# Kernel optimization log

Measured on AMD Instinct MI355X. Metric: run time of the kernel, lower is better.

The kernel has to match this reference:

```python
import jax, jax.numpy as jnp
import numpy as np

B, I, H = 32768, 1024, 1024

def _xavier(key, shape):
    fan_out, fan_in = shape
    limit = float(np.sqrt(6.0 / (fan_in + fan_out)))
    return jax.random.uniform(key, shape, jnp.float32, -limit, limit)

def setup_inputs() -> dict:
    key = jax.random.key(0)
    ks = jax.random.split(key, 8)
    return {
        "x": jax.random.normal(ks[0], (B, I), jnp.float32),
        "h": jax.random.normal(ks[1], (B, H), jnp.float32),
        "weight_ir": _xavier(ks[2], (H, I)),
        "weight_hr": _xavier(ks[3], (H, H)),
        "weight_iz": _xavier(ks[4], (H, I)),
        "weight_hz": _xavier(ks[5], (H, H)),
        "weight_in": _xavier(ks[6], (H, I)),
        "weight_hn": _xavier(ks[7], (H, H)),
        "bias_ir": jnp.zeros((H,), jnp.float32),
        "bias_hr": jnp.zeros((H,), jnp.float32),
        "bias_iz": jnp.zeros((H,), jnp.float32),
        "bias_hz": jnp.zeros((H,), jnp.float32),
        "bias_in": jnp.zeros((H,), jnp.float32),
        "bias_hn": jnp.zeros((H,), jnp.float32),
    }

def reference(x, h, weight_ir, weight_hr, weight_iz, weight_hz, weight_in, weight_hn,
              bias_ir, bias_hr, bias_iz, bias_hz, bias_in, bias_hn):
    # Fuse the 3 input-side and 3 hidden-side GEMMs into two concatenated GEMMs
    # (same math as 6 separate F.linear calls).
    Wi = jnp.concatenate([weight_ir, weight_iz, weight_in], axis=0)  # [3H, I]
    Wh = jnp.concatenate([weight_hr, weight_hz, weight_hn], axis=0)  # [3H, H]
    bi = jnp.concatenate([bias_ir, bias_iz, bias_in])
    bh = jnp.concatenate([bias_hr, bias_hz, bias_hn])
    gi = x @ Wi.T + bi   # [B, 3H]
    gh = h @ Wh.T + bh   # [B, 3H]
    Hd = weight_hr.shape[0]
    ir, iz, inn = gi[:, :Hd], gi[:, Hd:2*Hd], gi[:, 2*Hd:]
    hr, hz, hn = gh[:, :Hd], gh[:, Hd:2*Hd], gh[:, 2*Hd:]
    r = jax.nn.sigmoid(ir + hr)
    z = jax.nn.sigmoid(iz + hz)
    n = jnp.tanh(inn + r * hn)
    return (1.0 - z) * n + z * h
```

## Files before the change

### kernel.cpp

```cpp
#include <hip/hip_runtime.h>
#include <hip/hip_bf16.h>


#define B_ROWS 32768
#define KD     1024
#define HD     1024

#define BM 128
#define BN 64
#define BK 32

typedef __bf16 bf16_t;
typedef __bf16 bf16x8 __attribute__((ext_vector_type(8)));
typedef __bf16 bf16x4 __attribute__((ext_vector_type(4)));
typedef float  f32x4  __attribute__((ext_vector_type(4)));

#define XT_BYTES  67108864ull
#define WT_OFF   134217728ull
#define WS_NEEDED 146800640ull

#define X_SLOTS 4194304
#define W_BASE_SLOT 8388608
#define TOTAL_SLOTS 9175040

__device__ __forceinline__ float sigm_f(float v) { return 1.0f / (1.0f + __expf(-v)); }
__device__ __forceinline__ float tanh_f(float v) { return 2.0f / (1.0f + __expf(-2.0f * v)) - 1.0f; }

__device__ __forceinline__ bf16x4 cvt4(f32x4 v) {
    bf16x4 r;
    r[0] = (bf16_t)v[0]; r[1] = (bf16_t)v[1];
    r[2] = (bf16_t)v[2]; r[3] = (bf16_t)v[3];
    return r;
}

__device__ __forceinline__ void glds16(const void* g, void* l) {
    __builtin_amdgcn_global_load_lds(
        (const __attribute__((address_space(1))) void*)g,
        (__attribute__((address_space(3))) void*)l, 16, 0, 0);
}

struct WPtrs { const float* p[6]; };

__global__ void __launch_bounds__(256)
cvt_kernel(const float* __restrict__ x, const float* __restrict__ h,
           WPtrs wp, bf16_t* __restrict__ ws)
{
    int sid = blockIdx.x * 256 + threadIdx.x;
    if (sid >= TOTAL_SLOTS) return;

    const float* src;
    if (sid < W_BASE_SLOT) {
        const float* base = (sid < X_SLOTS) ? x : h;
        int s2   = sid & (X_SLOTS - 1);
        int tile = s2 >> 9;
        int c    = s2 & 511;
        int row  = c >> 2, s = c & 3;
        int mt   = tile >> 5, kt = tile & 31;
        int ks   = s ^ ((row >> 1) & 3);
        src = base + (size_t)(mt * 128 + row) * KD + kt * 32 + ks * 8;
    } else {
        int s2   = sid - W_BASE_SLOT;
        int tile = s2 / 1536;
        int c    = s2 % 1536;
        int g    = c >> 8;
        int cc   = c & 255;
        int row  = cc >> 2, s = cc & 3;
        int nt   = tile >> 5, kt = tile & 31;
        int ks   = s ^ ((row >> 1) & 3);
        src = wp.p[g] + (size_t)(nt * 64 + row) * KD + kt * 32 + ks * 8;
    }
    f32x4 a = *(const f32x4*)src;
    f32x4 b = *(const f32x4*)(src + 4);
    bf16x8 o;
    o[0]=(bf16_t)a[0]; o[1]=(bf16_t)a[1]; o[2]=(bf16_t)a[2]; o[3]=(bf16_t)a[3];
    o[4]=(bf16_t)b[0]; o[5]=(bf16_t)b[1]; o[6]=(bf16_t)b[2]; o[7]=(bf16_t)b[3];
    *(bf16x8*)(ws + (size_t)sid * 8) = o;
}

__global__ void __launch_bounds__(256, 2)
gru_mfma_kernel(const bf16_t* __restrict__ xt, const bf16_t* __restrict__ ht,
                const bf16_t* __restrict__ wt,
                const float* __restrict__ h,
                const float* __restrict__ b_ir, const float* __restrict__ b_hr,
                const float* __restrict__ b_iz, const float* __restrict__ b_hz,
                const float* __restrict__ b_in, const float* __restrict__ b_hn,
                float* __restrict__ out)
{
    __shared__ __align__(16) char smem[2][40960];

    const int tid  = threadIdx.x;
    const int lane = tid & 63;
    const int wid  = tid >> 6;
    const int wr   = wid >> 1;
    const int wc   = wid & 1;

    const int nblk = HD / BN;
    const int bidN = blockIdx.x % nblk;
    const int bidM = blockIdx.x / nblk;
    const int rowBase = bidM * BM;
    const int colBase = bidN * BN;

    const char* xcb = (const char*)xt + (size_t)bidM * 32 * 8192;
    const char* hcb = (const char*)ht + (size_t)bidM * 32 * 8192;
    const char* wcb = (const char*)wt + (size_t)bidN * 32 * 24576;

    const f32x4 vzero = {0.f, 0.f, 0.f, 0.f};
    f32x4 accR[4][2], accZ[4][2], accIN[4][2], accHN[4][2];
    #pragma unroll
    for (int m = 0; m < 4; ++m)
        #pragma unroll
        for (int n = 0; n < 2; ++n) {
            accR[m][n] = vzero; accZ[m][n] = vzero;
            accIN[m][n] = vzero; accHN[m][n] = vzero;
        }

    const int fr  = lane & 15;
    const int sl  = lane >> 4;
    const int f   = (fr >> 1) & 3;
    const int col = ((sl ^ f) << 4);
    int aoff[4], boff[2];
    #pragma unroll
    for (int m = 0; m < 4; ++m) aoff[m] = (wr * 64 + m * 16 + fr) * 64 + col;
    #pragma unroll
    for (int n = 0; n < 2; ++n) boff[n] = (wc * 32 + n * 16 + fr) * 64 + col;

    auto STAGE = [&](int buf, int kt) {
        const char* xc  = xcb + (size_t)kt * 8192;
        const char* hc  = hcb + (size_t)kt * 8192;
        const char* wc2 = wcb + (size_t)kt * 24576;
        char* s = smem[buf];
        #pragma unroll
        for (int i = 0; i < 2; ++i) {
            int off = wid * 2048 + i * 1024;
            glds16(xc + off + lane * 16, s + off);
            glds16(hc + off + lane * 16, s + 8192 + off);
        }
        #pragma unroll
        for (int j = 0; j < 6; ++j) {
            int off = wid * 6144 + j * 1024;
            glds16(wc2 + off + lane * 16, s + 16384 + off);
        }
    };

    auto COMPUTE = [&](const char* s) {
        bf16x8 xa[4], ha[4];
        #pragma unroll
        for (int m = 0; m < 4; ++m) {
            xa[m] = *(const bf16x8*)(s + aoff[m]);
            ha[m] = *(const bf16x8*)(s + 8192 + aoff[m]);
        }
        bf16x8 w0[2], w1[2];
        #pragma unroll
        for (int n = 0; n < 2; ++n) {
            w0[n] = *(const bf16x8*)(s + 16384 + 0 * 4096 + boff[n]);
            w1[n] = *(const bf16x8*)(s + 16384 + 1 * 4096 + boff[n]);
        }
        __builtin_amdgcn_s_setprio(1);
        #pragma unroll
        for (int m = 0; m < 4; ++m)
            #pragma unroll
            for (int n = 0; n < 2; ++n) {
                accR[m][n] = __builtin_amdgcn_mfma_f32_16x16x32_bf16(xa[m], w0[n], accR[m][n], 0, 0, 0);
                accR[m][n] = __builtin_amdgcn_mfma_f32_16x16x32_bf16(ha[m], w1[n], accR[m][n], 0, 0, 0);
            }
        __builtin_amdgcn_s_setprio(0);
        bf16x8 w2[2], w3[2];
        #pragma unroll
        for (int n = 0; n < 2; ++n) {
            w2[n] = *(const bf16x8*)(s + 16384 + 2 * 4096 + boff[n]);
            w3[n] = *(const bf16x8*)(s + 16384 + 3 * 4096 + boff[n]);
        }
        __builtin_amdgcn_s_setprio(1);
        #pragma unroll
        for (int m = 0; m < 4; ++m)
            #pragma unroll
            for (int n = 0; n < 2; ++n) {
                accZ[m][n] = __builtin_amdgcn_mfma_f32_16x16x32_bf16(xa[m], w2[n], accZ[m][n], 0, 0, 0);
                accZ[m][n] = __builtin_amdgcn_mfma_f32_16x16x32_bf16(ha[m], w3[n], accZ[m][n], 0, 0, 0);
            }
        __builtin_amdgcn_s_setprio(0);
        bf16x8 w4[2], w5[2];
        #pragma unroll
        for (int n = 0; n < 2; ++n) {
            w4[n] = *(const bf16x8*)(s + 16384 + 4 * 4096 + boff[n]);
            w5[n] = *(const bf16x8*)(s + 16384 + 5 * 4096 + boff[n]);
        }
        __builtin_amdgcn_s_setprio(1);
        #pragma unroll
        for (int m = 0; m < 4; ++m)
            #pragma unroll
            for (int n = 0; n < 2; ++n) {
                accIN[m][n] = __builtin_amdgcn_mfma_f32_16x16x32_bf16(xa[m], w4[n], accIN[m][n], 0, 0, 0);
                accHN[m][n] = __builtin_amdgcn_mfma_f32_16x16x32_bf16(ha[m], w5[n], accHN[m][n], 0, 0, 0);
            }
        __builtin_amdgcn_s_setprio(0);
    };

    STAGE(0, 0);

    for (int kt = 0; kt < 31; ++kt) {
        STAGE((kt + 1) & 1, kt + 1);
        asm volatile("s_waitcnt vmcnt(10)" ::: "memory");
        __builtin_amdgcn_s_barrier();
        __builtin_amdgcn_sched_barrier(0);
        COMPUTE(smem[kt & 1]);
        __builtin_amdgcn_sched_barrier(0);
        __builtin_amdgcn_s_barrier();
    }
    asm volatile("s_waitcnt vmcnt(0)" ::: "memory");
    __builtin_amdgcn_s_barrier();
    __builtin_amdgcn_sched_barrier(0);
    COMPUTE(smem[1]);

    const int rq = (lane >> 4) * 4;
    float br[2], bz[2], bi[2], bh[2];
    #pragma unroll
    for (int n = 0; n < 2; ++n) {
        int c = colBase + wc * 32 + n * 16 + fr;
        br[n] = b_ir[c] + b_hr[c];
        bz[n] = b_iz[c] + b_hz[c];
        bi[n] = b_in[c];
        bh[n] = b_hn[c];
    }
    #pragma unroll
    for (int m = 0; m < 4; ++m) {
        #pragma unroll
        for (int n = 0; n < 2; ++n) {
            int gc = colBase + wc * 32 + n * 16 + fr;
            #pragma unroll
            for (int j = 0; j < 4; ++j) {
                int gr = rowBase + wr * 64 + m * 16 + rq + j;
                float rv = sigm_f(accR[m][n][j] + br[n]);
                float zv = sigm_f(accZ[m][n][j] + bz[n]);
                float nv = tanh_f(accIN[m][n][j] + bi[n] + rv * (accHN[m][n][j] + bh[n]));
                float hv = h[(size_t)gr * HD + gc];
                out[(size_t)gr * HD + gc] = (1.0f - zv) * nv + zv * hv;
            }
        }
    }
}

#define PK 40
__global__ void __launch_bounds__(256, 2)
gru_fused_kernel(const float* __restrict__ x,  const float* __restrict__ h,
                 const float* __restrict__ w_ir, const float* __restrict__ w_hr,
                 const float* __restrict__ w_iz, const float* __restrict__ w_hz,
                 const float* __restrict__ w_in, const float* __restrict__ w_hn,
                 const float* __restrict__ b_ir, const float* __restrict__ b_hr,
                 const float* __restrict__ b_iz, const float* __restrict__ b_hz,
                 const float* __restrict__ b_in, const float* __restrict__ b_hn,
                 float* __restrict__ out)
{
    __shared__ __align__(16) bf16_t xs[BM][PK];
    __shared__ __align__(16) bf16_t hs[BM][PK];
    __shared__ __align__(16) bf16_t ws[6][BN][PK];

    const int tid  = threadIdx.x;
    const int lane = tid & 63;
    const int wid  = tid >> 6;
    const int wr   = wid >> 1;
    const int wc   = wid & 1;

    const int nblk = HD / BN;
    const int bidN = blockIdx.x % nblk;
    const int bidM = blockIdx.x / nblk;
    const int rowBase = bidM * BM;
    const int colBase = bidN * BN;

    const float* wptr[6] = { w_ir, w_hr, w_iz, w_hz, w_in, w_hn };

    int sr[4], sc[4];
    #pragma unroll
    for (int i = 0; i < 4; ++i) {
        int idx = tid + i * 256;
        sr[i] = idx >> 3;
        sc[i] = (idx & 7) * 4;
    }
    int xoff[4];
    #pragma unroll
    for (int i = 0; i < 4; ++i) xoff[i] = (rowBase + sr[i]) * KD + sc[i];
    int woff[2];
    #pragma unroll
    for (int i = 0; i < 2; ++i) woff[i] = (colBase + sr[i]) * KD + sc[i];

    const f32x4 vzero = {0.f, 0.f, 0.f, 0.f};
    f32x4 accR[4][2], accZ[4][2], accIN[4][2], accHN[4][2];
    #pragma unroll
    for (int m = 0; m < 4; ++m)
        #pragma unroll
        for (int n = 0; n < 2; ++n) {
            accR[m][n] = vzero; accZ[m][n] = vzero;
            accIN[m][n] = vzero; accHN[m][n] = vzero;
        }

    const int fr = lane & 15;
    const int ko = (lane >> 4) * 8;

    for (int k0 = 0; k0 < KD; k0 += BK) {
        __syncthreads();
        #pragma unroll
        for (int i = 0; i < 4; ++i) {
            f32x4 vx = *(const f32x4*)&x[xoff[i] + k0];
            f32x4 vh = *(const f32x4*)&h[xoff[i] + k0];
            *(bf16x4*)&xs[sr[i]][sc[i]] = cvt4(vx);
            *(bf16x4*)&hs[sr[i]][sc[i]] = cvt4(vh);
        }
        #pragma unroll
        for (int g = 0; g < 6; ++g) {
            #pragma unroll
            for (int i = 0; i < 2; ++i) {
                f32x4 vw = *(const f32x4*)&wptr[g][woff[i] + k0];
                *(bf16x4*)&ws[g][sr[i]][sc[i]] = cvt4(vw);
            }
        }
        __syncthreads();

        bf16x8 xa[4], ha[4];
        #pragma unroll
        for (int m = 0; m < 4; ++m) {
            xa[m] = *(const bf16x8*)&xs[wr * 64 + m * 16 + fr][ko];
            ha[m] = *(const bf16x8*)&hs[wr * 64 + m * 16 + fr][ko];
        }
        bf16x8 wb[6][2];
        #pragma unroll
        for (int g = 0; g < 6; ++g)
            #pragma unroll
            for (int n = 0; n < 2; ++n)
                wb[g][n] = *(const bf16x8*)&ws[g][wc * 32 + n * 16 + fr][ko];

        #pragma unroll
        for (int m = 0; m < 4; ++m) {
            #pragma unroll
            for (int n = 0; n < 2; ++n) {
                accR[m][n]  = __builtin_amdgcn_mfma_f32_16x16x32_bf16(xa[m], wb[0][n], accR[m][n], 0, 0, 0);
                accR[m][n]  = __builtin_amdgcn_mfma_f32_16x16x32_bf16(ha[m], wb[1][n], accR[m][n], 0, 0, 0);
                accZ[m][n]  = __builtin_amdgcn_mfma_f32_16x16x32_bf16(xa[m], wb[2][n], accZ[m][n], 0, 0, 0);
                accZ[m][n]  = __builtin_amdgcn_mfma_f32_16x16x32_bf16(ha[m], wb[3][n], accZ[m][n], 0, 0, 0);
                accIN[m][n] = __builtin_amdgcn_mfma_f32_16x16x32_bf16(xa[m], wb[4][n], accIN[m][n], 0, 0, 0);
                accHN[m][n] = __builtin_amdgcn_mfma_f32_16x16x32_bf16(ha[m], wb[5][n], accHN[m][n], 0, 0, 0);
            }
        }
    }

    const int rq = (lane >> 4) * 4;
    float br[2], bz[2], bi[2], bh[2];
    #pragma unroll
    for (int n = 0; n < 2; ++n) {
        int c = colBase + wc * 32 + n * 16 + fr;
        br[n] = b_ir[c] + b_hr[c];
        bz[n] = b_iz[c] + b_hz[c];
        bi[n] = b_in[c];
        bh[n] = b_hn[c];
    }
    #pragma unroll
    for (int m = 0; m < 4; ++m) {
        #pragma unroll
        for (int n = 0; n < 2; ++n) {
            int gc = colBase + wc * 32 + n * 16 + fr;
            #pragma unroll
            for (int j = 0; j < 4; ++j) {
                int gr = rowBase + wr * 64 + m * 16 + rq + j;
                float rv = sigm_f(accR[m][n][j] + br[n]);
                float zv = sigm_f(accZ[m][n][j] + bz[n]);
                float nv = tanh_f(accIN[m][n][j] + bi[n] + rv * (accHN[m][n][j] + bh[n]));
                float hv = h[gr * HD + gc];
                out[gr * HD + gc] = (1.0f - zv) * nv + zv * hv;
            }
        }
    }
}

extern "C" void kernel_launch(void* const* d_in, const int* in_sizes, int n_in,
                              void* d_out, int out_size, void* d_ws, size_t ws_size,
                              hipStream_t stream) {
    const float* x    = (const float*)d_in[0];
    const float* h    = (const float*)d_in[1];
    const float* w_ir = (const float*)d_in[2];
    const float* w_hr = (const float*)d_in[3];
    const float* w_iz = (const float*)d_in[4];
    const float* w_hz = (const float*)d_in[5];
    const float* w_in = (const float*)d_in[6];
    const float* w_hn = (const float*)d_in[7];
    const float* b_ir = (const float*)d_in[8];
    const float* b_hr = (const float*)d_in[9];
    const float* b_iz = (const float*)d_in[10];
    const float* b_hz = (const float*)d_in[11];
    const float* b_in = (const float*)d_in[12];
    const float* b_hn = (const float*)d_in[13];
    float* out = (float*)d_out;

    if (ws_size >= WS_NEEDED) {
        bf16_t* ws = (bf16_t*)d_ws;
        WPtrs wp;
        wp.p[0] = w_ir; wp.p[1] = w_hr; wp.p[2] = w_iz;
        wp.p[3] = w_hz; wp.p[4] = w_in; wp.p[5] = w_hn;
        cvt_kernel<<<(TOTAL_SLOTS + 255) / 256, 256, 0, stream>>>(x, h, wp, ws);

        const bf16_t* xt = ws;
        const bf16_t* ht = ws + XT_BYTES / 2;
        const bf16_t* wt = ws + WT_OFF / 2;
        dim3 grid((B_ROWS / BM) * (HD / BN));
        gru_mfma_kernel<<<grid, 256, 0, stream>>>(
            xt, ht, wt, h, b_ir, b_hr, b_iz, b_hz, b_in, b_hn, out);
    } else {
        dim3 grid((B_ROWS / BM) * (HD / BN));
        gru_fused_kernel<<<grid, 256, 0, stream>>>(
            x, h, w_ir, w_hr, w_iz, w_hz, w_in, w_hn,
            b_ir, b_hr, b_iz, b_hz, b_in, b_hn, out);
    }
}
```

Baseline: 477.4 us.

## Widen MFMA GRU tile to 128x128 with 8 waves and inner-loop barriers

Doubles the N tile of the bf16 MFMA GRU kernel to 128 columns and runs it with 512 threads (8 waves, 2x4 layout), so each staged x/h tile is reused across twice as many output columns and global traffic for the activations is halved. The weight pre-conversion layout is changed to match the 128-row weight tiles. The compute body is inlined into the loop, with explicit lgkmcnt waits and extra workgroup barriers between the gate phases. The trade-off is 128KB of LDS per block, one block per CU, and more barriers, which lowers latency hiding and occupancy.

```diff
diff --git a/kernel.cpp b/kernel.cpp
--- a/kernel.cpp
+++ b/kernel.cpp
@@ -7,7 +7,7 @@
 #define HD     1024
 
 #define BM 128
-#define BN 64
+#define BN 128
 #define BK 32
 
 typedef __bf16 bf16_t;
@@ -60,14 +60,14 @@
         src = base + (size_t)(mt * 128 + row) * KD + kt * 32 + ks * 8;
     } else {
         int s2   = sid - W_BASE_SLOT;
-        int tile = s2 / 1536;
-        int c    = s2 % 1536;
-        int g    = c >> 8;
-        int cc   = c & 255;
+        int tile = s2 / 3072;
+        int c    = s2 % 3072;
+        int g    = c >> 9;
+        int cc   = c & 511;
         int row  = cc >> 2, s = cc & 3;
         int nt   = tile >> 5, kt = tile & 31;
         int ks   = s ^ ((row >> 1) & 3);
-        src = wp.p[g] + (size_t)(nt * 64 + row) * KD + kt * 32 + ks * 8;
+        src = wp.p[g] + (size_t)(nt * 128 + row) * KD + kt * 32 + ks * 8;
     }
     f32x4 a = *(const f32x4*)src;
     f32x4 b = *(const f32x4*)(src + 4);
@@ -77,7 +77,7 @@
     *(bf16x8*)(ws + (size_t)sid * 8) = o;
 }
 
-__global__ void __launch_bounds__(256, 2)
+__global__ void __launch_bounds__(512, 1)
 gru_mfma_kernel(const bf16_t* __restrict__ xt, const bf16_t* __restrict__ ht,
                 const bf16_t* __restrict__ wt,
                 const float* __restrict__ h,
@@ -86,13 +86,13 @@
                 const float* __restrict__ b_in, const float* __restrict__ b_hn,
                 float* __restrict__ out)
 {
-    __shared__ __align__(16) char smem[2][40960];
+    __shared__ __align__(16) char smem[2][65536];
 
     const int tid  = threadIdx.x;
     const int lane = tid & 63;
     const int wid  = tid >> 6;
-    const int wr   = wid >> 1;
-    const int wc   = wid & 1;
+    const int wrM  = wid >> 2;
+    const int wcN  = wid & 3;
 
     const int nblk = HD / BN;
     const int bidN = blockIdx.x % nblk;
@@ -102,7 +102,7 @@
 
     const char* xcb = (const char*)xt + (size_t)bidM * 32 * 8192;
     const char* hcb = (const char*)ht + (size_t)bidM * 32 * 8192;
-    const char* wcb = (const char*)wt + (size_t)bidN * 32 * 24576;
+    const char* wcb = (const char*)wt + (size_t)bidN * 32 * 49152;
 
     const f32x4 vzero = {0.f, 0.f, 0.f, 0.f};
     f32x4 accR[4][2], accZ[4][2], accIN[4][2], accHN[4][2];
@@ -120,29 +120,32 @@
     const int col = ((sl ^ f) << 4);
     int aoff[4], boff[2];
     #pragma unroll
-    for (int m = 0; m < 4; ++m) aoff[m] = (wr * 64 + m * 16 + fr) * 64 + col;
-    #pragma unroll
-    for (int n = 0; n < 2; ++n) boff[n] = (wc * 32 + n * 16 + fr) * 64 + col;
+    for (int m = 0; m < 4; ++m) aoff[m] = (wrM * 64 + m * 16 + fr) * 64 + col;
+    #pragma unroll
+    for (int n = 0; n < 2; ++n) boff[n] = (wcN * 32 + n * 16 + fr) * 64 + col;
 
     auto STAGE = [&](int buf, int kt) {
         const char* xc  = xcb + (size_t)kt * 8192;
         const char* hc  = hcb + (size_t)kt * 8192;
-        const char* wc2 = wcb + (size_t)kt * 24576;
+        const char* wc2 = wcb + (size_t)kt * 49152;
         char* s = smem[buf];
-        #pragma unroll
-        for (int i = 0; i < 2; ++i) {
-            int off = wid * 2048 + i * 1024;
-            glds16(xc + off + lane * 16, s + off);
-            glds16(hc + off + lane * 16, s + 8192 + off);
-        }
-        #pragma unroll
-        for (int j = 0; j < 6; ++j) {
-            int off = wid * 6144 + j * 1024;
-            glds16(wc2 + off + lane * 16, s + 16384 + off);
-        }
+        const int wo = wid * 1024;
+        glds16(xc + wo + lane * 16, s + wo);
+        glds16(hc + wo + lane * 16, s + 8192 + wo);
+        #pragma unroll
+        for (int g = 0; g < 6; ++g)
+            glds16(wc2 + g * 8192 + wo + lane * 16, s + 16384 + g * 8192 + wo);
     };
 
-    auto COMPUTE = [&](const char* s) {
+    STAGE(0, 0);
+
+    for (int kt = 0; kt < 31; ++kt) {
+        STAGE((kt + 1) & 1, kt + 1);
+        asm volatile("s_waitcnt vmcnt(8)" ::: "memory");
+        __builtin_amdgcn_s_barrier();
+        __builtin_amdgcn_sched_barrier(0);
+        const char* s = smem[kt & 1];
+
         bf16x8 xa[4], ha[4];
         #pragma unroll
         for (int m = 0; m < 4; ++m) {
@@ -152,9 +155,11 @@
         bf16x8 w0[2], w1[2];
         #pragma unroll
         for (int n = 0; n < 2; ++n) {
-            w0[n] = *(const bf16x8*)(s + 16384 + 0 * 4096 + boff[n]);
-            w1[n] = *(const bf16x8*)(s + 16384 + 1 * 4096 + boff[n]);
-        }
+            w0[n] = *(const bf16x8*)(s + 16384 + 0 * 8192 + boff[n]);
+            w1[n] = *(const bf16x8*)(s + 16384 + 1 * 8192 + boff[n]);
+        }
+        asm volatile("s_waitcnt lgkmcnt(0)" ::: "memory");
+        __builtin_amdgcn_sched_barrier(0);
         __builtin_amdgcn_s_setprio(1);
         #pragma unroll
         for (int m = 0; m < 4; ++m)
@@ -164,12 +169,16 @@
                 accR[m][n] = __builtin_amdgcn_mfma_f32_16x16x32_bf16(ha[m], w1[n], accR[m][n], 0, 0, 0);
             }
         __builtin_amdgcn_s_setprio(0);
+        __builtin_amdgcn_s_barrier();
+
         bf16x8 w2[2], w3[2];
         #pragma unroll
         for (int n = 0; n < 2; ++n) {
-            w2[n] = *(const bf16x8*)(s + 16384 + 2 * 4096 + boff[n]);
-            w3[n] = *(const bf16x8*)(s + 16384 + 3 * 4096 + boff[n]);
-        }
+            w2[n] = *(const bf16x8*)(s + 16384 + 2 * 8192 + boff[n]);
+            w3[n] = *(const bf16x8*)(s + 16384 + 3 * 8192 + boff[n]);
+        }
+        asm volatile("s_waitcnt lgkmcnt(0)" ::: "memory");
+        __builtin_amdgcn_sched_barrier(0);
         __builtin_amdgcn_s_setprio(1);
         #pragma unroll
         for (int m = 0; m < 4; ++m)
@@ -179,12 +188,16 @@
                 accZ[m][n] = __builtin_amdgcn_mfma_f32_16x16x32_bf16(ha[m], w3[n], accZ[m][n], 0, 0, 0);
             }
         __builtin_amdgcn_s_setprio(0);
+        __builtin_amdgcn_s_barrier();
+
         bf16x8 w4[2], w5[2];
         #pragma unroll
         for (int n = 0; n < 2; ++n) {
-            w4[n] = *(const bf16x8*)(s + 16384 + 4 * 4096 + boff[n]);
-            w5[n] = *(const bf16x8*)(s + 16384 + 5 * 4096 + boff[n]);
-        }
+            w4[n] = *(const bf16x8*)(s + 16384 + 4 * 8192 + boff[n]);
+            w5[n] = *(const bf16x8*)(s + 16384 + 5 * 8192 + boff[n]);
+        }
+        asm volatile("s_waitcnt lgkmcnt(0)" ::: "memory");
+        __builtin_amdgcn_sched_barrier(0);
         __builtin_amdgcn_s_setprio(1);
         #pragma unroll
         for (int m = 0; m < 4; ++m)
@@ -194,29 +207,45 @@
                 accHN[m][n] = __builtin_amdgcn_mfma_f32_16x16x32_bf16(ha[m], w5[n], accHN[m][n], 0, 0, 0);
             }
         __builtin_amdgcn_s_setprio(0);
-    };
-
-    STAGE(0, 0);
-
-    for (int kt = 0; kt < 31; ++kt) {
-        STAGE((kt + 1) & 1, kt + 1);
-        asm volatile("s_waitcnt vmcnt(10)" ::: "memory");
         __builtin_amdgcn_s_barrier();
-        __builtin_amdgcn_sched_barrier(0);
-        COMPUTE(smem[kt & 1]);
-        __builtin_amdgcn_sched_barrier(0);
+    }
+
+    {
+        asm volatile("s_waitcnt vmcnt(0)" ::: "memory");
         __builtin_amdgcn_s_barrier();
-    }
-    asm volatile("s_waitcnt vmcnt(0)" ::: "memory");
-    __builtin_amdgcn_s_barrier();
-    __builtin_amdgcn_sched_barrier(0);
-    COMPUTE(smem[1]);
+        __builtin_amdgcn_sched_barrier(0);
+        const char* s = smem[1];
+        bf16x8 xa[4], ha[4], wb[6][2];
+        #pragma unroll
+        for (int m = 0; m < 4; ++m) {
+            xa[m] = *(const bf16x8*)(s + aoff[m]);
+            ha[m] = *(const bf16x8*)(s + 8192 + aoff[m]);
+        }
+        #pragma unroll
+        for (int g = 0; g < 6; ++g)
+            #pragma unroll
+            for (int n = 0; n < 2; ++n)
+                wb[g][n] = *(const bf16x8*)(s + 16384 + g * 8192 + boff[n]);
+        asm volatile("s_waitcnt lgkmcnt(0)" ::: "memory");
+        __builtin_amdgcn_sched_barrier(0);
+        #pragma unroll
+        for (int m = 0; m < 4; ++m)
+            #pragma unroll
+            for (int n = 0; n < 2; ++n) {
+                accR[m][n]  = __builtin_amdgcn_mfma_f32_16x16x32_bf16(xa[m], wb[0][n], accR[m][n], 0, 0, 0);
+                accR[m][n]  = __builtin_amdgcn_mfma_f32_16x16x32_bf16(ha[m], wb[1][n], accR[m][n], 0, 0, 0);
+                accZ[m][n]  = __builtin_amdgcn_mfma_f32_16x16x32_bf16(xa[m], wb[2][n], accZ[m][n], 0, 0, 0);
+                accZ[m][n]  = __builtin_amdgcn_mfma_f32_16x16x32_bf16(ha[m], wb[3][n], accZ[m][n], 0, 0, 0);
+                accIN[m][n] = __builtin_amdgcn_mfma_f32_16x16x32_bf16(xa[m], wb[4][n], accIN[m][n], 0, 0, 0);
+                accHN[m][n] = __builtin_amdgcn_mfma_f32_16x16x32_bf16(ha[m], wb[5][n], accHN[m][n], 0, 0, 0);
+            }
+    }
 
     const int rq = (lane >> 4) * 4;
     float br[2], bz[2], bi[2], bh[2];
     #pragma unroll
     for (int n = 0; n < 2; ++n) {
-        int c = colBase + wc * 32 + n * 16 + fr;
+        int c = colBase + wcN * 32 + n * 16 + fr;
         br[n] = b_ir[c] + b_hr[c];
         bz[n] = b_iz[c] + b_hz[c];
         bi[n] = b_in[c];
@@ -226,10 +255,10 @@
     for (int m = 0; m < 4; ++m) {
         #pragma unroll
         for (int n = 0; n < 2; ++n) {
-            int gc = colBase + wc * 32 + n * 16 + fr;
+            int gc = colBase + wcN * 32 + n * 16 + fr;
             #pragma unroll
             for (int j = 0; j < 4; ++j) {
-                int gr = rowBase + wr * 64 + m * 16 + rq + j;
+                int gr = rowBase + wrM * 64 + m * 16 + rq + j;
                 float rv = sigm_f(accR[m][n][j] + br[n]);
                 float zv = sigm_f(accZ[m][n][j] + bz[n]);
                 float nv = tanh_f(accIN[m][n][j] + bi[n] + rv * (accHN[m][n][j] + bh[n]));
@@ -241,6 +270,8 @@
 }
 
 #define PK 40
+#define FBM 128
+#define FBN 64
 __global__ void __launch_bounds__(256, 2)
 gru_fused_kernel(const float* __restrict__ x,  const float* __restrict__ h,
                  const float* __restrict__ w_ir, const float* __restrict__ w_hr,
@@ -251,9 +282,9 @@
                  const float* __restrict__ b_in, const float* __restrict__ b_hn,
                  float* __restrict__ out)
 {
-    __shared__ __align__(16) bf16_t xs[BM][PK];
-    __shared__ __align__(16) bf16_t hs[BM][PK];
-    __shared__ __align__(16) bf16_t ws[6][BN][PK];
+    __shared__ __align__(16) bf16_t xs[FBM][PK];
+    __shared__ __align__(16) bf16_t hs[FBM][PK];
+    __shared__ __align__(16) bf16_t ws[6][FBN][PK];
 
     const int tid  = threadIdx.x;
     const int lane = tid & 63;
@@ -261,11 +292,11 @@
     const int wr   = wid >> 1;
     const int wc   = wid & 1;
 
-    const int nblk = HD / BN;
+    const int nblk = HD / FBN;
     const int bidN = blockIdx.x % nblk;
     const int bidM = blockIdx.x / nblk;
-    const int rowBase = bidM * BM;
-    const int colBase = bidN * BN;
+    const int rowBase = bidM * FBM;
+    const int colBase = bidN * FBN;
 
     const float* wptr[6] = { w_ir, w_hr, w_iz, w_hz, w_in, w_hn };
 
@@ -400,10 +431,10 @@
         const bf16_t* ht = ws + XT_BYTES / 2;
         const bf16_t* wt = ws + WT_OFF / 2;
         dim3 grid((B_ROWS / BM) * (HD / BN));
-        gru_mfma_kernel<<<grid, 256, 0, stream>>>(
+        gru_mfma_kernel<<<grid, 512, 0, stream>>>(
             xt, ht, wt, h, b_ir, b_hr, b_iz, b_hz, b_in, b_hn, out);
     } else {
-        dim3 grid((B_ROWS / BM) * (HD / BN));
+        dim3 grid((B_ROWS / FBM) * (HD / FBN));
         gru_fused_kernel<<<grid, 256, 0, stream>>>(
             x, h, w_ir, w_hr, w_iz, w_hz, w_in, w_hn,
             b_ir, b_hr, b_iz, b_hz, b_in, b_hn, out);
```

Measured after the change: 573.0 us. +20.0%, slower.
